# Optimization experiments

Hardware: AMD Instinct MI355X
Metric: run time of the kernel (lower is better)

The kernel has to match this reference:

```python
import jax, jax.numpy as jnp
import numpy as np

DEPTH = 8            # max(code_depth)
CODE_DEPTH = (1, 8)  # (vqgan_depth, vqkd_depth)
N_EMBED = 8192
EMBED_DIM = 64
B, H, W = 32, 32, 32


def setup_inputs() -> dict:
    key = jax.random.key(0)
    kx, kc = jax.random.split(key)
    x = jax.random.normal(kx, (B, EMBED_DIM, H, W), dtype=jnp.float32)
    # 8 codebooks, each (n_embed, embed_dim); torch nn.Embedding init is N(0,1)
    codebooks = jax.random.normal(kc, (DEPTH, N_EMBED, EMBED_DIM), dtype=jnp.float32)
    return {"x": x, "codebooks": codebooks}


def _quantize(x_code, codebooks):
    # x_code: (B, h, w, d) -- already stop-gradient'd (torch clones a detached copy)
    b, h, w, d = x_code.shape
    xf = x_code.reshape(-1, d)  # (N, d)

    def step(carry, cb):
        residual, agg = carry
        # squared L2 distances via ||r||^2 + ||c||^2 - 2 r c^T  (torch addmm)
        r_sq = jnp.sum(residual * residual, axis=1, keepdims=True)      # (N, 1)
        c_sq = jnp.sum(cb * cb, axis=1)[None, :]                         # (1, K)
        dist = r_sq + c_sq - 2.0 * (residual @ cb.T)                     # (N, K)
        code = jnp.argmin(dist, axis=1)                                  # (N,)
        quant = cb[code]                                                 # (N, d)
        d_norm = jnp.mean(jnp.sum(dist * dist, axis=-1))
        residual = residual - quant
        agg = agg + quant
        return (residual, agg), (agg, code, d_norm)

    (_, _), (quants, codes, d_norms) = jax.lax.scan(
        step, (xf, jnp.zeros_like(xf)), codebooks)
    quants = quants.reshape(DEPTH, b, h, w, d)             # cumulative quants
    codes = jnp.transpose(codes.reshape(DEPTH, b, h, w), (1, 2, 3, 0))  # (B,h,w,DEPTH)
    return quants, codes, d_norms


def reference(x, codebooks):
    x_code = jnp.transpose(x, (0, 2, 3, 1))  # b c h w -> b h w c
    quants, codes, d_norms = _quantize(jax.lax.stop_gradient(x_code), codebooks)
    # commitment loss: mean over depth of mean((x - agg_quant.detach())^2)
    commit_loss = jnp.mean((x_code[None] - jax.lax.stop_gradient(quants)) ** 2)
    # straight-through outputs in latent (b c h w) shape
    vqkd = jnp.transpose(quants[CODE_DEPTH[1] - 1], (0, 3, 1, 2))
    vqkd_zq = x + jax.lax.stop_gradient(vqkd - x)
    vqgan = jnp.transpose(quants[CODE_DEPTH[0] - 1], (0, 3, 1, 2))
    vqgan_zq = x + jax.lax.stop_gradient(vqgan - x)
    vqkd_d_norm = d_norms[CODE_DEPTH[1] - 1]
    vqgan_d_norm = d_norms[CODE_DEPTH[0] - 1]
    return (vqgan_zq, vqkd_zq, commit_loss, vqkd_d_norm, vqgan_d_norm, codes)
```

## Files before the change

kernel.cpp:

```cpp
#include <hip/hip_runtime.h>

#define OFF_RES    0u
#define OFF_BH     8388608u
#define OFF_BL     9437184u
#define OFF_CSQD   10485760u
#define OFF_CSQH   11010048u
#define OFF_CODES  11272192u
#define OFF_PM1    11403264u
#define OFF_PM2    12451840u
#define OFF_PI1    13500416u
#define OFF_FLAG   14548992u
#define OFF_M0     14680064u
#define OFF_M7     14712832u
#define OFF_DNP    14745600u
#define OFF_FCNT   14749696u
#define OFF_PCOM   14749760u
#define OFF_PDN    15274048u

#define TAU 3.0e-3f

typedef __attribute__((ext_vector_type(8))) _Float16 f16x8;
typedef __attribute__((ext_vector_type(4))) float f32x4;

__device__ __forceinline__ f32x4 mfma16(f16x8 a, f16x8 b, f32x4 c) {
  return __builtin_amdgcn_mfma_f32_16x16x32_f16(a, b, c, 0, 0, 0);
}

__global__ __launch_bounds__(256) void srq_transpose_init(
    const float* __restrict__ x, float* __restrict__ resid)
{
  __shared__ float tile[64][65];
  const int b   = blockIdx.x >> 4;
  const int hw0 = (blockIdx.x & 15) << 6;
  const int t = threadIdx.x;
#pragma unroll
  for (int i = 0; i < 16; ++i) {
    int e = i * 256 + t;
    int c = e >> 6, hw = e & 63;
    tile[c][hw] = x[(size_t)b * 65536 + (size_t)c * 1024 + hw0 + hw];
  }
  __syncthreads();
#pragma unroll
  for (int i = 0; i < 16; ++i) {
    int e = i * 256 + t;
    int hw = e >> 6, c = e & 63;
    resid[((size_t)(b * 1024 + hw0 + hw) << 6) + c] = tile[c][hw];
  }
}

__global__ __launch_bounds__(256) void srq_csq(
    const float* __restrict__ cb, double* __restrict__ csqD, float* __restrict__ csqH)
{
  int id = blockIdx.x * 256 + threadIdx.x;
  const float* p = cb + ((size_t)id << 6);
  double s = 0.0;
#pragma unroll 8
  for (int d = 0; d < 64; ++d) { double v = (double)p[d]; s = fma(v, v, s); }
  csqD[id] = s;
  csqH[id] = (float)(-0.5 * s);
}

__global__ __launch_bounds__(256) void srq_bconv(
    const float* __restrict__ cb, _Float16* __restrict__ Bh, _Float16* __restrict__ Bl)
{
  int id0 = (blockIdx.x * 256 + threadIdx.x) * 4;
  float4 v = *(const float4*)(cb + id0);
  const float f[4] = {v.x, v.y, v.z, v.w};
#pragma unroll
  for (int u = 0; u < 4; ++u) {
    _Float16 h = (_Float16)f[u];
    Bh[id0 + u] = h;
    Bl[id0 + u] = (_Float16)((f[u] - (float)h) * 2048.f);
  }
}

__global__ __launch_bounds__(256) void srq_dnpre_partial(
    const float* __restrict__ cb, const double* __restrict__ csqD,
    double* __restrict__ Pm, double* __restrict__ Ps1, double* __restrict__ Ps2)
{
  __shared__ float ch[32][64];
  const int t = threadIdx.x;
  const int b = blockIdx.x;
  const int i = t >> 2;
  const int j0 = (t & 3) << 4;
  double acc[16];
#pragma unroll
  for (int n = 0; n < 16; ++n) acc[n] = 0.0;
  double s1 = 0.0, s2 = 0.0;
  for (int c8 = 0; c8 < 8; ++c8) {
    const int kbase = b * 256 + c8 * 32;
    __syncthreads();
    const float* src = cb + (size_t)kbase * 64;
#pragma unroll
    for (int u = 0; u < 2; ++u)
      *(float4*)(&ch[0][0] + (u * 256 + t) * 4) = *(const float4*)(src + (u * 256 + t) * 4);
    __syncthreads();
#pragma unroll 4
    for (int kk = 0; kk < 32; ++kk) {
      double ci = (double)ch[kk][i];
#pragma unroll
      for (int n = 0; n < 16; ++n)
        acc[n] = fma(ci, (double)ch[kk][j0 + n], acc[n]);
    }
    if (t < 64) {
#pragma unroll 4
      for (int kk = 0; kk < 32; ++kk) {
        double v = (double)ch[kk][t];
        s1 += v;
        s2 = fma(csqD[kbase + kk], v, s2);
      }
    }
  }
  double* dst = Pm + ((size_t)b << 12) + (i << 6) + j0;
#pragma unroll
  for (int n = 0; n < 16; ++n) dst[n] = acc[n];
  if (t < 64) { Ps1[(b << 6) + t] = s1; Ps2[(b << 6) + t] = s2; }
}

__global__ __launch_bounds__(256) void srq_dnpre_reduce(
    const double* __restrict__ Pm, const double* __restrict__ Ps1,
    const double* __restrict__ Ps2, const double* __restrict__ csqD,
    double* __restrict__ Mmat, double* __restrict__ S1, double* __restrict__ S2,
    double* __restrict__ CS)
{
  const int t = threadIdx.x;
  if (blockIdx.x < 16) {
    const int e = blockIdx.x * 256 + t;
    double a = 0.0;
    for (int b = 0; b < 32; ++b) a += Pm[((size_t)b << 12) + e];
    Mmat[e] = a;
  } else {
    __shared__ double red[256];
    if (t < 64) {
      double a1 = 0.0, a2 = 0.0;
      for (int b = 0; b < 32; ++b) { a1 += Ps1[(b << 6) + t]; a2 += Ps2[(b << 6) + t]; }
      S1[t] = a1; S2[t] = a2;
    }
    double c1 = 0.0, c2 = 0.0;
    for (int k = t; k < 8192; k += 256) { double q = csqD[k]; c1 += q; c2 = fma(q, q, c2); }
    red[t] = c1;
    __syncthreads();
    for (int o = 128; o; o >>= 1) { if (t < o) red[t] += red[t + o]; __syncthreads(); }
    if (t == 0) CS[0] = red[0];
    __syncthreads();
    red[t] = c2;
    __syncthreads();
    for (int o = 128; o; o >>= 1) { if (t < o) red[t] += red[t + o]; __syncthreads(); }
    if (t == 0) CS[1] = red[0];
  }
}

__device__ __forceinline__ void stage_tile(
    const _Float16* __restrict__ Bh, const _Float16* __restrict__ Bl,
    char* ldsbase, int k0, int wid, int lane)
{
#pragma unroll
  for (int q = 0; q < 4; ++q) {
    int ub = (((q << 2) + wid) << 10);
    int db = ub + lane * 16;
    int half = db >> 13;
    int rowh = (db & 8191) >> 7;
    int soff = (db & 127) ^ ((rowh & 7) << 4);
    const _Float16* g = (half ? Bl : Bh) + (((size_t)(k0 + rowh)) << 6) + (soff >> 1);
    __builtin_amdgcn_global_load_lds(
        (const __attribute__((address_space(1))) void*)g,
        (__attribute__((address_space(3))) void*)(ldsbase + ub), 16, 0, 0);
  }
}

__global__ __launch_bounds__(256, 3) void srq_screen_mfma(
    const _Float16* __restrict__ Bh, const _Float16* __restrict__ Bl,
    const float* __restrict__ csqH, const float* __restrict__ resid,
    float* __restrict__ pm1, float* __restrict__ pm2, int* __restrict__ pi1)
{
  __shared__ char lds[32768];
  const int tid = threadIdx.x;
  const int lane = tid & 63;
  const int wid = tid >> 6;
  const int rg = blockIdx.x & 255;
  const int ks = blockIdx.x >> 8;
  const int k0g = ks << 10;
  const int wrow0 = (rg << 7) + (wid << 5);
  const int lr = lane & 15;
  const int kg = lane >> 4;

  f16x8 ah[2][2], al[2][2];
#pragma unroll
  for (int rf = 0; rf < 2; ++rf)
#pragma unroll
    for (int s = 0; s < 2; ++s) {
      const float* rp = resid + (((size_t)(wrow0 + rf * 16 + lr)) << 6) + s * 32 + kg * 8;
      float4 v0 = *(const float4*)rp;
      float4 v1 = *(const float4*)(rp + 4);
      float f[8] = {v0.x, v0.y, v0.z, v0.w, v1.x, v1.y, v1.z, v1.w};
      f16x8 h, l;
#pragma unroll
      for (int e = 0; e < 8; ++e) {
        _Float16 hh = (_Float16)f[e];
        h[e] = hh;
        l[e] = (_Float16)((f[e] - (float)hh) * 2048.f);
      }
      ah[rf][s] = h;
      al[rf][s] = l;
    }

  float m1[8], m2[8];
  int i1[8];
#pragma unroll
  for (int j = 0; j < 8; ++j) { m1[j] = -3e38f; m2[j] = -3e38f; i1[j] = 0; }

  stage_tile(Bh, Bl, lds, k0g, wid, lane);

  for (int t = 0; t < 16; ++t) {
    __syncthreads();
    if (t < 15) stage_tile(Bh, Bl, lds + (((t + 1) & 1) << 14), k0g + ((t + 1) << 6), wid, lane);
    const char* bb = lds + ((t & 1) << 14);
    const int k0 = k0g + (t << 6);
#pragma unroll
    for (int cf = 0; cf < 4; ++cf) {
      const int cl = cf * 16 + lr;
      const int sw = (cl & 7) << 4;
      const int ro = cl * 128 + kg * 16;
      f16x8 bh0 = *(const f16x8*)(bb + ((ro) ^ sw));
      f16x8 bh1 = *(const f16x8*)(bb + ((ro + 64) ^ sw));
      f16x8 bl0 = *(const f16x8*)(bb + 8192 + ((ro) ^ sw));
      f16x8 bl1 = *(const f16x8*)(bb + 8192 + ((ro + 64) ^ sw));
      const int code = k0 + cl;
      const float ci = csqH[code];
#pragma unroll
      for (int rf = 0; rf < 2; ++rf) {
        f32x4 a1 = {ci, ci, ci, ci};
        f32x4 a2 = {0.f, 0.f, 0.f, 0.f};
        a1 = mfma16(ah[rf][0], bh0, a1);
        a1 = mfma16(ah[rf][1], bh1, a1);
        a2 = mfma16(ah[rf][0], bl0, a2);
        a2 = mfma16(al[rf][0], bh0, a2);
        a2 = mfma16(ah[rf][1], bl1, a2);
        a2 = mfma16(al[rf][1], bh1, a2);
#pragma unroll
        for (int r = 0; r < 4; ++r) {
          float sg = fmaf(4.8828125e-4f, a2[r], a1[r]);
          const int j = rf * 4 + r;
          bool gt = sg > m1[j];
          m2[j] = __builtin_amdgcn_fmed3f(sg, m1[j], m2[j]);
          m1[j] = fmaxf(m1[j], sg);
          i1[j] = gt ? code : i1[j];
        }
      }
    }
  }

#pragma unroll
  for (int j = 0; j < 8; ++j) {
    float a1 = m1[j], a2 = m2[j];
    int ai = i1[j];
#pragma unroll
    for (int w = 1; w <= 8; w <<= 1) {
      float b1 = __shfl_xor(a1, w);
      float b2 = __shfl_xor(a2, w);
      int bi = __shfl_xor(ai, w);
      float nm2 = fmaxf(fminf(a1, b1), fmaxf(a2, b2));
      bool bet = (b1 > a1) || (b1 == a1 && bi < ai);
      a1 = fmaxf(a1, b1);
      ai = bet ? bi : ai;
      a2 = nm2;
    }
    if (lr == 0) {
      const int row = wrow0 + (j >> 2) * 16 + kg * 4 + (j & 3);
      pm1[row * 8 + ks] = -2.f * a1;
      pm2[row * 8 + ks] = -2.f * a2;
      pi1[row * 8 + ks] = ai;
    }
  }
}

__global__ __launch_bounds__(256) void srq_merge_row(
    const float* __restrict__ pm1, const float* __restrict__ pm2,
    const int* __restrict__ pi1, int* __restrict__ codes,
    int* __restrict__ flagList, int* __restrict__ flagCnt)
{
  const int row = blockIdx.x * 256 + threadIdx.x;
  const float* p1 = pm1 + row * 8;
  const float* p2 = pm2 + row * 8;
  const int*   pv = pi1 + row * 8;
  float m1 = p1[0], m2 = p2[0];
  int ii = pv[0];
#pragma unroll
  for (int k = 1; k < 8; ++k) {
    float b1 = p1[k], b2 = p2[k];
    int bi = pv[k];
    m2 = fminf(fmaxf(m1, b1), fminf(m2, b2));
    if (b1 < m1) { m1 = b1; ii = bi; }
  }
  codes[row] = ii;
  if (m2 - m1 < TAU) {
    int pos = atomicAdd(flagCnt, 1);
    flagList[pos] = row;
  }
}

__global__ __launch_bounds__(256) void srq_refine(
    const float* __restrict__ cb, const double* __restrict__ csqD,
    const float* __restrict__ resid, int* __restrict__ codes,
    const int* __restrict__ flagList, const int* __restrict__ flagCnt)
{
  __shared__ float rowv[64];
  __shared__ double vals[256];
  __shared__ int   idxs[256];
  int cnt = *flagCnt;
  for (int j = blockIdx.x; j < cnt; j += gridDim.x) {
    int row = flagList[j];
    __syncthreads();
    if (threadIdx.x < 64) rowv[threadIdx.x] = resid[((size_t)row << 6) + threadIdx.x];
    __syncthreads();
    double bv = 1e300;
    int bi = 0x7fffffff;
    for (int i = 0; i < 32; ++i) {
      int k = i * 256 + threadIdx.x;
      const float* cp = cb + ((size_t)k << 6);
      double a0 = 0.0, a1 = 0.0, a2 = 0.0, a3 = 0.0;
#pragma unroll
      for (int d = 0; d < 64; d += 4) {
        a0 = fma((double)rowv[d    ], (double)cp[d    ], a0);
        a1 = fma((double)rowv[d + 1], (double)cp[d + 1], a1);
        a2 = fma((double)rowv[d + 2], (double)cp[d + 2], a2);
        a3 = fma((double)rowv[d + 3], (double)cp[d + 3], a3);
      }
      double s = csqD[k] - 2.0 * ((a0 + a1) + (a2 + a3));
      if (s < bv) { bv = s; bi = k; }
    }
    vals[threadIdx.x] = bv;
    idxs[threadIdx.x] = bi;
    __syncthreads();
    if (threadIdx.x == 0) {
      double g = vals[0]; int gi = idxs[0];
      for (int u = 1; u < 256; ++u) {
        if (vals[u] < g || (vals[u] == g && idxs[u] < gi)) { g = vals[u]; gi = idxs[u]; }
      }
      codes[row] = gi;
    }
    __syncthreads();
  }
}

template <int NEED_DN>
__global__ __launch_bounds__(256) void srq_update(
    const float* __restrict__ cb, float* __restrict__ resid,
    const int* __restrict__ codes, float* __restrict__ codesF,
    double* __restrict__ Pcom, double* __restrict__ Pdn,
    const double* __restrict__ Mmat, const double* __restrict__ S1v,
    const double* __restrict__ S2v, const double* __restrict__ CS,
    const float* __restrict__ cbNext, _Float16* __restrict__ BhN,
    _Float16* __restrict__ BlN, int dep)
{
  __shared__ double w4[4];
  __shared__ double d4[4];
  const int t = threadIdx.x;
  const int team = t >> 6;
  const int c = t & 63;

  if (cbNext) {
    int gid = blockIdx.x * 512 + t;
#pragma unroll
    for (int u = 0; u < 2; ++u) {
      int g2 = gid + u * 256;
      float v = cbNext[g2];
      _Float16 h = (_Float16)v;
      BhN[g2] = h;
      BlN[g2] = (_Float16)((v - (float)h) * 2048.f);
    }
  }

  int rows[8], cds[8];
#pragma unroll
  for (int g = 0; g < 8; ++g) {
    rows[g] = (blockIdx.x * 8 + g) * 4 + team;
    cds[g] = codes[rows[g]];
  }
  float rpre[8], qv[8];
#pragma unroll
  for (int g = 0; g < 8; ++g) rpre[g] = resid[((size_t)rows[g] << 6) + c];
#pragma unroll
  for (int g = 0; g < 8; ++g) qv[g] = cb[((size_t)cds[g] << 6) + c];

  double com = 0.0, dnSum = 0.0;
#pragma unroll
  for (int g = 0; g < 8; ++g) {
    float r = rpre[g] - qv[g];
    resid[((size_t)rows[g] << 6) + c] = r;
    float p = r * r;
#pragma unroll
    for (int o = 32; o; o >>= 1) p += __shfl_down(p, o);
    if (c == 0) {
      codesF[(size_t)rows[g] * 8 + dep] = (float)cds[g];
      com += (double)p;
    }
  }

  if (NEED_DN) {
#pragma unroll 1
    for (int g = 0; g < 8; ++g) {
      const double rc = (double)rpre[g];
      double mr = 0.0;
#pragma unroll 4
      for (int i = 0; i < 64; ++i)
        mr = fma(Mmat[i * 64 + c], (double)__shfl(rpre[g], i), mr);
      double qm = mr * rc;
      double av = rc * S1v[c];
      double b2 = rc * S2v[c];
      double r2 = rc * rc;
#pragma unroll
      for (int o = 32; o; o >>= 1) {
        qm += __shfl_down(qm, o);
        av += __shfl_down(av, o);
        b2 += __shfl_down(b2, o);
        r2 += __shfl_down(r2, o);
      }
      if (c == 0)
        dnSum += 8192.0 * r2 * r2 + CS[1] + 4.0 * qm
               + 2.0 * r2 * CS[0] - 4.0 * r2 * av - 4.0 * b2;
    }
  }

  if (c == 0) { w4[team] = com; d4[team] = dnSum; }
  __syncthreads();
  if (t == 0) Pcom[blockIdx.x] = (w4[0] + w4[1]) + (w4[2] + w4[3]);
  if (NEED_DN && t == 1) Pdn[blockIdx.x] = (d4[0] + d4[1]) + (d4[2] + d4[3]);
}

__global__ __launch_bounds__(256) void srq_writeout(
    const float* __restrict__ x, const float* __restrict__ resid, float* __restrict__ out)
{
  __shared__ float tile[64][65];
  const int b   = blockIdx.x >> 4;
  const int hw0 = (blockIdx.x & 15) << 6;
  const int t = threadIdx.x;
#pragma unroll
  for (int i = 0; i < 16; ++i) {
    int e = i * 256 + t;
    int hw = e >> 6, c = e & 63;
    tile[hw][c] = resid[((size_t)(b * 1024 + hw0 + hw) << 6) + c];
  }
  __syncthreads();
#pragma unroll
  for (int i = 0; i < 16; ++i) {
    int e = i * 256 + t;
    int c = e >> 6, hw = e & 63;
    size_t o = (size_t)b * 65536 + (size_t)c * 1024 + hw0 + hw;
    out[o] = x[o] - tile[hw][c];
  }
}

__global__ __launch_bounds__(256) void srq_finalize(
    const double* __restrict__ Pcom, const double* __restrict__ Pdn,
    float* __restrict__ outs)
{
  __shared__ double red[256];
  const int t = threadIdx.x;
  double s = 0.0;
  for (int i = t; i < 8192; i += 256) s += Pcom[i];
  red[t] = s;
  __syncthreads();
  for (int o = 128; o; o >>= 1) { if (t < o) red[t] += red[t + o]; __syncthreads(); }
  const double commit = red[0];
  __syncthreads();
  s = 0.0;
  for (int i = t; i < 1024; i += 256) s += Pdn[i];
  red[t] = s;
  __syncthreads();
  for (int o = 128; o; o >>= 1) { if (t < o) red[t] += red[t + o]; __syncthreads(); }
  const double dn0 = red[0];
  __syncthreads();
  s = 0.0;
  for (int i = t; i < 1024; i += 256) s += Pdn[1024 + i];
  red[t] = s;
  __syncthreads();
  for (int o = 128; o; o >>= 1) { if (t < o) red[t] += red[t + o]; __syncthreads(); }
  if (t == 0) {
    outs[0] = (float)(commit / 16777216.0);
    outs[1] = (float)(red[0] / 32768.0);
    outs[2] = (float)(dn0 / 32768.0);
  }
}

extern "C" void kernel_launch(void* const* d_in, const int* in_sizes, int n_in,
                              void* d_out, int out_size, void* d_ws, size_t ws_size,
                              hipStream_t stream) {
  const float* x  = (const float*)d_in[0];
  const float* cb = (const float*)d_in[1];
  char* ws = (char*)d_ws;

  float*  resid = (float*)(ws + OFF_RES);
  _Float16* Bh  = (_Float16*)(ws + OFF_BH);
  _Float16* Bl  = (_Float16*)(ws + OFF_BL);
  double* csqD  = (double*)(ws + OFF_CSQD);
  float*  csqH  = (float*)(ws + OFF_CSQH);
  int*    codes = (int*)(ws + OFF_CODES);
  float*  pm1   = (float*)(ws + OFF_PM1);
  float*  pm2   = (float*)(ws + OFF_PM2);
  int*    pi1   = (int*)(ws + OFF_PI1);
  int*    flags = (int*)(ws + OFF_FLAG);
  double* M0    = (double*)(ws + OFF_M0);
  double* M7    = (double*)(ws + OFF_M7);
  double* S1_0  = (double*)(ws + OFF_DNP);
  double* S2_0  = (double*)(ws + OFF_DNP + 512);
  double* S1_7  = (double*)(ws + OFF_DNP + 1024);
  double* S2_7  = (double*)(ws + OFF_DNP + 1536);
  double* CS0   = (double*)(ws + OFF_DNP + 2048);
  double* CS7   = (double*)(ws + OFF_DNP + 2064);
  int*    fcnt  = (int*)(ws + OFF_FCNT);
  double* Pcom  = (double*)(ws + OFF_PCOM);
  double* Pdn   = (double*)(ws + OFF_PDN);

  double* Pm  = (double*)(ws + OFF_PM1);
  double* Ps1 = (double*)(ws + OFF_PM2);
  double* Ps2 = (double*)(ws + OFF_PI1);

  float* out_vqgan = (float*)d_out;
  float* out_vqkd  = out_vqgan + 2097152;
  float* out_scal  = out_vqgan + 4194304;
  float* out_codes = out_vqgan + 4194307;

  hipMemsetAsync(ws + OFF_FCNT, 0, 32, stream);
  srq_transpose_init<<<512, 256, 0, stream>>>(x, resid);
  srq_csq<<<256, 256, 0, stream>>>(cb, csqD, csqH);
  srq_dnpre_partial<<<32, 256, 0, stream>>>(cb, csqD, Pm, Ps1, Ps2);
  srq_dnpre_reduce<<<17, 256, 0, stream>>>(Pm, Ps1, Ps2, csqD, M0, S1_0, S2_0, CS0);
  srq_dnpre_partial<<<32, 256, 0, stream>>>(cb + (size_t)7 * 524288, csqD + 7 * 8192,
                                            Pm, Ps1, Ps2);
  srq_dnpre_reduce<<<17, 256, 0, stream>>>(Pm, Ps1, Ps2, csqD + 7 * 8192,
                                           M7, S1_7, S2_7, CS7);
  srq_bconv<<<512, 256, 0, stream>>>(cb, Bh, Bl);

  for (int dep = 0; dep < 8; ++dep) {
    const float* cbd = cb + (size_t)dep * 524288;
    const float* cbn = (dep < 7) ? cb + (size_t)(dep + 1) * 524288 : nullptr;
    srq_screen_mfma<<<2048, 256, 0, stream>>>(Bh, Bl, csqH + dep * 8192, resid, pm1, pm2, pi1);
    srq_merge_row<<<128, 256, 0, stream>>>(pm1, pm2, pi1, codes, flags, fcnt + dep);
    srq_refine<<<128, 256, 0, stream>>>(cbd, csqD + dep * 8192, resid, codes,
                                        flags, fcnt + dep);
    if (dep == 0 || dep == 7) {
      srq_update<1><<<1024, 256, 0, stream>>>(cbd, resid, codes, out_codes,
          Pcom + (size_t)dep * 1024, Pdn + (dep == 0 ? 0 : 1024),
          (dep == 0 ? M0 : M7), (dep == 0 ? S1_0 : S1_7),
          (dep == 0 ? S2_0 : S2_7), (dep == 0 ? CS0 : CS7),
          cbn, Bh, Bl, dep);
    } else {
      srq_update<0><<<1024, 256, 0, stream>>>(cbd, resid, codes, out_codes,
          Pcom + (size_t)dep * 1024, nullptr,
          nullptr, nullptr, nullptr, nullptr,
          cbn, Bh, Bl, dep);
    }
    if (dep == 0) srq_writeout<<<512, 256, 0, stream>>>(x, resid, out_vqgan);
    if (dep == 7) srq_writeout<<<512, 256, 0, stream>>>(x, resid, out_vqkd);
  }
  srq_finalize<<<1, 256, 0, stream>>>(Pcom, Pdn, out_scal);
}
```

Measured before the change: 1.856 ms.

## Fuse merge, refine and residual update into one post-screen kernel

Replaces the separate merge_row, refine and update kernels with one kernel launch per depth. The first 1024 blocks merge partial minima in-wave and update residuals for unflagged rows. The extra 128 blocks each merge their own rows, build a block-local flagged list via ballot, and do exact fp64 refinement plus residual update for those rows. This removes two launches per depth, the global atomic flag counter and its memset, and the codes buffer round-trip. The cost is that refine blocks run serially over their flagged rows inside one launch and may become the tail.

```diff
diff --git a/kernel.cpp b/kernel.cpp
--- a/kernel.cpp
+++ b/kernel.cpp
@@ -5,15 +5,12 @@
 #define OFF_BL     9437184u
 #define OFF_CSQD   10485760u
 #define OFF_CSQH   11010048u
-#define OFF_CODES  11272192u
 #define OFF_PM1    11403264u
 #define OFF_PM2    12451840u
 #define OFF_PI1    13500416u
-#define OFF_FLAG   14548992u
 #define OFF_M0     14680064u
 #define OFF_M7     14712832u
 #define OFF_DNP    14745600u
-#define OFF_FCNT   14749696u
 #define OFF_PCOM   14749760u
 #define OFF_PDN    15274048u
 
@@ -274,158 +271,188 @@
   }
 }
 
-__global__ __launch_bounds__(256) void srq_merge_row(
+template <int NEED_DN>
+__global__ __launch_bounds__(256) void srq_post(
     const float* __restrict__ pm1, const float* __restrict__ pm2,
-    const int* __restrict__ pi1, int* __restrict__ codes,
-    int* __restrict__ flagList, int* __restrict__ flagCnt)
-{
-  const int row = blockIdx.x * 256 + threadIdx.x;
-  const float* p1 = pm1 + row * 8;
-  const float* p2 = pm2 + row * 8;
-  const int*   pv = pi1 + row * 8;
-  float m1 = p1[0], m2 = p2[0];
-  int ii = pv[0];
-#pragma unroll
-  for (int k = 1; k < 8; ++k) {
-    float b1 = p1[k], b2 = p2[k];
-    int bi = pv[k];
-    m2 = fminf(fmaxf(m1, b1), fminf(m2, b2));
-    if (b1 < m1) { m1 = b1; ii = bi; }
-  }
-  codes[row] = ii;
-  if (m2 - m1 < TAU) {
-    int pos = atomicAdd(flagCnt, 1);
-    flagList[pos] = row;
-  }
-}
-
-__global__ __launch_bounds__(256) void srq_refine(
-    const float* __restrict__ cb, const double* __restrict__ csqD,
-    const float* __restrict__ resid, int* __restrict__ codes,
-    const int* __restrict__ flagList, const int* __restrict__ flagCnt)
-{
-  __shared__ float rowv[64];
-  __shared__ double vals[256];
-  __shared__ int   idxs[256];
-  int cnt = *flagCnt;
-  for (int j = blockIdx.x; j < cnt; j += gridDim.x) {
-    int row = flagList[j];
-    __syncthreads();
-    if (threadIdx.x < 64) rowv[threadIdx.x] = resid[((size_t)row << 6) + threadIdx.x];
-    __syncthreads();
-    double bv = 1e300;
-    int bi = 0x7fffffff;
-    for (int i = 0; i < 32; ++i) {
-      int k = i * 256 + threadIdx.x;
-      const float* cp = cb + ((size_t)k << 6);
-      double a0 = 0.0, a1 = 0.0, a2 = 0.0, a3 = 0.0;
-#pragma unroll
-      for (int d = 0; d < 64; d += 4) {
-        a0 = fma((double)rowv[d    ], (double)cp[d    ], a0);
-        a1 = fma((double)rowv[d + 1], (double)cp[d + 1], a1);
-        a2 = fma((double)rowv[d + 2], (double)cp[d + 2], a2);
-        a3 = fma((double)rowv[d + 3], (double)cp[d + 3], a3);
-      }
-      double s = csqD[k] - 2.0 * ((a0 + a1) + (a2 + a3));
-      if (s < bv) { bv = s; bi = k; }
-    }
-    vals[threadIdx.x] = bv;
-    idxs[threadIdx.x] = bi;
-    __syncthreads();
-    if (threadIdx.x == 0) {
-      double g = vals[0]; int gi = idxs[0];
-      for (int u = 1; u < 256; ++u) {
-        if (vals[u] < g || (vals[u] == g && idxs[u] < gi)) { g = vals[u]; gi = idxs[u]; }
-      }
-      codes[row] = gi;
-    }
-    __syncthreads();
-  }
-}
-
-template <int NEED_DN>
-__global__ __launch_bounds__(256) void srq_update(
-    const float* __restrict__ cb, float* __restrict__ resid,
-    const int* __restrict__ codes, float* __restrict__ codesF,
+    const int* __restrict__ pi1, const float* __restrict__ cb,
+    const double* __restrict__ csqD,
+    float* __restrict__ resid, float* __restrict__ codesF,
     double* __restrict__ Pcom, double* __restrict__ Pdn,
     const double* __restrict__ Mmat, const double* __restrict__ S1v,
     const double* __restrict__ S2v, const double* __restrict__ CS,
     const float* __restrict__ cbNext, _Float16* __restrict__ BhN,
     _Float16* __restrict__ BlN, int dep)
 {
-  __shared__ double w4[4];
-  __shared__ double d4[4];
   const int t = threadIdx.x;
-  const int team = t >> 6;
-  const int c = t & 63;
-
-  if (cbNext) {
-    int gid = blockIdx.x * 512 + t;
-#pragma unroll
-    for (int u = 0; u < 2; ++u) {
-      int g2 = gid + u * 256;
-      float v = cbNext[g2];
-      _Float16 h = (_Float16)v;
-      BhN[g2] = h;
-      BlN[g2] = (_Float16)((v - (float)h) * 2048.f);
-    }
-  }
-
-  int rows[8], cds[8];
-#pragma unroll
-  for (int g = 0; g < 8; ++g) {
-    rows[g] = (blockIdx.x * 8 + g) * 4 + team;
-    cds[g] = codes[rows[g]];
-  }
-  float rpre[8], qv[8];
-#pragma unroll
-  for (int g = 0; g < 8; ++g) rpre[g] = resid[((size_t)rows[g] << 6) + c];
-#pragma unroll
-  for (int g = 0; g < 8; ++g) qv[g] = cb[((size_t)cds[g] << 6) + c];
-
-  double com = 0.0, dnSum = 0.0;
-#pragma unroll
-  for (int g = 0; g < 8; ++g) {
-    float r = rpre[g] - qv[g];
-    resid[((size_t)rows[g] << 6) + c] = r;
-    float p = r * r;
-#pragma unroll
-    for (int o = 32; o; o >>= 1) p += __shfl_down(p, o);
-    if (c == 0) {
-      codesF[(size_t)rows[g] * 8 + dep] = (float)cds[g];
-      com += (double)p;
-    }
-  }
-
-  if (NEED_DN) {
-#pragma unroll 1
+
+  if (blockIdx.x < 1024) {
+    __shared__ double w4[4];
+    __shared__ double d4[4];
+    const int b = blockIdx.x;
+    const int team = t >> 6;
+    const int c = t & 63;
+    const int row0 = b * 32 + team * 8;
+
+    if (cbNext) {
+      int gid = b * 512 + t;
+#pragma unroll
+      for (int u = 0; u < 2; ++u) {
+        int g2 = gid + u * 256;
+        float v = cbNext[g2];
+        _Float16 h = (_Float16)v;
+        BhN[g2] = h;
+        BlN[g2] = (_Float16)((v - (float)h) * 2048.f);
+      }
+    }
+
+    const int mrow = row0 + (c >> 3);
+    float a1 = pm1[mrow * 8 + (c & 7)];
+    float a2 = pm2[mrow * 8 + (c & 7)];
+    int ai = pi1[mrow * 8 + (c & 7)];
+#pragma unroll
+    for (int w = 1; w <= 4; w <<= 1) {
+      float b1 = __shfl_xor(a1, w);
+      float b2 = __shfl_xor(a2, w);
+      int bi = __shfl_xor(ai, w);
+      float nm2 = fminf(fmaxf(a1, b1), fminf(a2, b2));
+      bool bet = (b1 < a1) || (b1 == a1 && bi < ai);
+      a1 = fminf(a1, b1);
+      ai = bet ? bi : ai;
+      a2 = nm2;
+    }
+    const int myflag = (a2 - a1 < TAU) ? 1 : 0;
+
+    float rpre[8];
+#pragma unroll
+    for (int g = 0; g < 8; ++g) rpre[g] = resid[((size_t)(row0 + g) << 6) + c];
+
+    double com = 0.0, dnSum = 0.0;
+#pragma unroll
     for (int g = 0; g < 8; ++g) {
-      const double rc = (double)rpre[g];
-      double mr = 0.0;
+      const int code_g = __shfl(ai, g << 3);
+      const int flag_g = __shfl(myflag, g << 3);
+      if (!flag_g) {
+        float q = cb[((size_t)code_g << 6) + c];
+        float r = rpre[g] - q;
+        resid[((size_t)(row0 + g) << 6) + c] = r;
+        float p = r * r;
+#pragma unroll
+        for (int o = 32; o; o >>= 1) p += __shfl_down(p, o);
+        if (c == 0) {
+          codesF[(size_t)(row0 + g) * 8 + dep] = (float)code_g;
+          com += (double)p;
+        }
+      }
+      if (NEED_DN) {
+        const double rc = (double)rpre[g];
+        double mr = 0.0;
 #pragma unroll 4
-      for (int i = 0; i < 64; ++i)
-        mr = fma(Mmat[i * 64 + c], (double)__shfl(rpre[g], i), mr);
-      double qm = mr * rc;
-      double av = rc * S1v[c];
-      double b2 = rc * S2v[c];
-      double r2 = rc * rc;
-#pragma unroll
-      for (int o = 32; o; o >>= 1) {
-        qm += __shfl_down(qm, o);
-        av += __shfl_down(av, o);
-        b2 += __shfl_down(b2, o);
-        r2 += __shfl_down(r2, o);
-      }
-      if (c == 0)
-        dnSum += 8192.0 * r2 * r2 + CS[1] + 4.0 * qm
-               + 2.0 * r2 * CS[0] - 4.0 * r2 * av - 4.0 * b2;
-    }
-  }
-
-  if (c == 0) { w4[team] = com; d4[team] = dnSum; }
-  __syncthreads();
-  if (t == 0) Pcom[blockIdx.x] = (w4[0] + w4[1]) + (w4[2] + w4[3]);
-  if (NEED_DN && t == 1) Pdn[blockIdx.x] = (d4[0] + d4[1]) + (d4[2] + d4[3]);
+        for (int i = 0; i < 64; ++i)
+          mr = fma(Mmat[i * 64 + c], (double)__shfl(rpre[g], i), mr);
+        double qm = mr * rc;
+        double av = rc * S1v[c];
+        double b2 = rc * S2v[c];
+        double r2 = rc * rc;
+#pragma unroll
+        for (int o = 32; o; o >>= 1) {
+          qm += __shfl_down(qm, o);
+          av += __shfl_down(av, o);
+          b2 += __shfl_down(b2, o);
+          r2 += __shfl_down(r2, o);
+        }
+        if (c == 0)
+          dnSum += 8192.0 * r2 * r2 + CS[1] + 4.0 * qm
+                 + 2.0 * r2 * CS[0] - 4.0 * r2 * av - 4.0 * b2;
+      }
+    }
+    if (c == 0) { w4[team] = com; d4[team] = dnSum; }
+    __syncthreads();
+    if (t == 0) Pcom[b] = (w4[0] + w4[1]) + (w4[2] + w4[3]);
+    if (NEED_DN && t == 1) Pdn[b] = (d4[0] + d4[1]) + (d4[2] + d4[3]);
+  } else {
+    __shared__ int list[256];
+    __shared__ int wcnt[4];
+    __shared__ int lcnt;
+    __shared__ float rowv[64];
+    __shared__ double vals[256];
+    __shared__ int idxs[256];
+    __shared__ int sbest;
+    const int rb = blockIdx.x - 1024;
+    const int row = rb * 256 + t;
+
+    const float* p1 = pm1 + row * 8;
+    const float* p2 = pm2 + row * 8;
+    const int* pv = pi1 + row * 8;
+    float m1 = p1[0], m2 = p2[0];
+    int ii = pv[0];
+#pragma unroll
+    for (int k = 1; k < 8; ++k) {
+      float b1 = p1[k], b2 = p2[k];
+      int bi = pv[k];
+      m2 = fminf(fmaxf(m1, b1), fminf(m2, b2));
+      if (b1 < m1) { m1 = b1; ii = bi; }
+    }
+    const bool flagged = (m2 - m1 < TAU);
+
+    unsigned long long mask = __ballot(flagged);
+    const int lane = t & 63;
+    const int wid = t >> 6;
+    if (lane == 0) wcnt[wid] = __popcll(mask);
+    __syncthreads();
+    int base = 0;
+    for (int w = 0; w < wid; ++w) base += wcnt[w];
+    if (flagged) list[base + __popcll(mask & ((1ull << lane) - 1ull))] = row;
+    if (t == 0) lcnt = wcnt[0] + wcnt[1] + wcnt[2] + wcnt[3];
+    __syncthreads();
+    const int cnt = lcnt;
+
+    double com = 0.0;
+    for (int j = 0; j < cnt; ++j) {
+      const int frow = list[j];
+      __syncthreads();
+      if (t < 64) rowv[t] = resid[((size_t)frow << 6) + t];
+      __syncthreads();
+      double bv = 1e300;
+      int bi = 0x7fffffff;
+      for (int i = 0; i < 32; ++i) {
+        int k = i * 256 + t;
+        const float* cp = cb + ((size_t)k << 6);
+        double a0 = 0.0, a1d = 0.0, a2d = 0.0, a3d = 0.0;
+#pragma unroll
+        for (int d = 0; d < 64; d += 4) {
+          a0  = fma((double)rowv[d    ], (double)cp[d    ], a0);
+          a1d = fma((double)rowv[d + 1], (double)cp[d + 1], a1d);
+          a2d = fma((double)rowv[d + 2], (double)cp[d + 2], a2d);
+          a3d = fma((double)rowv[d + 3], (double)cp[d + 3], a3d);
+        }
+        double s = csqD[k] - 2.0 * ((a0 + a1d) + (a2d + a3d));
+        if (s < bv) { bv = s; bi = k; }
+      }
+      vals[t] = bv;
+      idxs[t] = bi;
+      __syncthreads();
+      if (t == 0) {
+        double g = vals[0]; int gi = idxs[0];
+        for (int u = 1; u < 256; ++u) {
+          if (vals[u] < g || (vals[u] == g && idxs[u] < gi)) { g = vals[u]; gi = idxs[u]; }
+        }
+        sbest = gi;
+        codesF[(size_t)frow * 8 + dep] = (float)gi;
+      }
+      __syncthreads();
+      if (t < 64) {
+        float q = cb[((size_t)sbest << 6) + t];
+        float r = rowv[t] - q;
+        resid[((size_t)frow << 6) + t] = r;
+        float p = r * r;
+#pragma unroll
+        for (int o = 32; o; o >>= 1) p += __shfl_down(p, o);
+        if (t == 0) com += (double)p;
+      }
+      __syncthreads();
+    }
+    if (t == 0) Pcom[1024 + rb] = com;
+  }
 }
 
 __global__ __launch_bounds__(256) void srq_writeout(
@@ -458,7 +485,7 @@
   __shared__ double red[256];
   const int t = threadIdx.x;
   double s = 0.0;
-  for (int i = t; i < 8192; i += 256) s += Pcom[i];
+  for (int i = t; i < 9216; i += 256) s += Pcom[i];
   red[t] = s;
   __syncthreads();
   for (int o = 128; o; o >>= 1) { if (t < o) red[t] += red[t + o]; __syncthreads(); }
@@ -495,11 +522,9 @@
   _Float16* Bl  = (_Float16*)(ws + OFF_BL);
   double* csqD  = (double*)(ws + OFF_CSQD);
   float*  csqH  = (float*)(ws + OFF_CSQH);
-  int*    codes = (int*)(ws + OFF_CODES);
   float*  pm1   = (float*)(ws + OFF_PM1);
   float*  pm2   = (float*)(ws + OFF_PM2);
   int*    pi1   = (int*)(ws + OFF_PI1);
-  int*    flags = (int*)(ws + OFF_FLAG);
   double* M0    = (double*)(ws + OFF_M0);
   double* M7    = (double*)(ws + OFF_M7);
   double* S1_0  = (double*)(ws + OFF_DNP);
@@ -508,7 +533,6 @@
   double* S2_7  = (double*)(ws + OFF_DNP + 1536);
   double* CS0   = (double*)(ws + OFF_DNP + 2048);
   double* CS7   = (double*)(ws + OFF_DNP + 2064);
-  int*    fcnt  = (int*)(ws + OFF_FCNT);
   double* Pcom  = (double*)(ws + OFF_PCOM);
   double* Pdn   = (double*)(ws + OFF_PDN);
 
@@ -521,7 +545,6 @@
   float* out_scal  = out_vqgan + 4194304;
   float* out_codes = out_vqgan + 4194307;
 
-  hipMemsetAsync(ws + OFF_FCNT, 0, 32, stream);
   srq_transpose_init<<<512, 256, 0, stream>>>(x, resid);
   srq_csq<<<256, 256, 0, stream>>>(cb, csqD, csqH);
   srq_dnpre_partial<<<32, 256, 0, stream>>>(cb, csqD, Pm, Ps1, Ps2);
@@ -536,18 +559,15 @@
     const float* cbd = cb + (size_t)dep * 524288;
     const float* cbn = (dep < 7) ? cb + (size_t)(dep + 1) * 524288 : nullptr;
     srq_screen_mfma<<<2048, 256, 0, stream>>>(Bh, Bl, csqH + dep * 8192, resid, pm1, pm2, pi1);
-    srq_merge_row<<<128, 256, 0, stream>>>(pm1, pm2, pi1, codes, flags, fcnt + dep);
-    srq_refine<<<128, 256, 0, stream>>>(cbd, csqD + dep * 8192, resid, codes,
-                                        flags, fcnt + dep);
     if (dep == 0 || dep == 7) {
-      srq_update<1><<<1024, 256, 0, stream>>>(cbd, resid, codes, out_codes,
-          Pcom + (size_t)dep * 1024, Pdn + (dep == 0 ? 0 : 1024),
+      srq_post<1><<<1152, 256, 0, stream>>>(pm1, pm2, pi1, cbd, csqD + dep * 8192,
+          resid, out_codes, Pcom + (size_t)dep * 1152, Pdn + (dep == 0 ? 0 : 1024),
           (dep == 0 ? M0 : M7), (dep == 0 ? S1_0 : S1_7),
           (dep == 0 ? S2_0 : S2_7), (dep == 0 ? CS0 : CS7),
           cbn, Bh, Bl, dep);
     } else {
-      srq_update<0><<<1024, 256, 0, stream>>>(cbd, resid, codes, out_codes,
-          Pcom + (size_t)dep * 1024, nullptr,
+      srq_post<0><<<1152, 256, 0, stream>>>(pm1, pm2, pi1, cbd, csqD + dep * 8192,
+          resid, out_codes, Pcom + (size_t)dep * 1152, nullptr,
           nullptr, nullptr, nullptr, nullptr,
           cbn, Bh, Bl, dep);
     }
```

New measurement: 2.391 ms. 28.8% more time.
